# Optimization experiments

Measured on AMD Instinct MI355X. Metric: run time of the kernel, lower is better.

## Reference

```python
import jax, jax.numpy as jnp
import numpy as np
import math

B = 1024
FV = 4096
E = 256
Z = E + 1
EPS = 1e-3
INNER_NSTEP = 8
INNER_LR = 0.5
NS = 16


def setup_inputs() -> dict:
    key = jax.random.key(0)
    ks = jax.random.split(key, 6)
    img = jax.random.uniform(ks[0], (B, FV), dtype=jnp.float32)
    lab = jax.random.randint(ks[1], (B,), 0, 10, dtype=jnp.int64)
    w_dec_w = jax.random.normal(ks[2], (FV, E), dtype=jnp.float32) / np.sqrt(E)
    w_dec_b = jnp.zeros((FV,), dtype=jnp.float32)
    whz_w = jax.random.normal(ks[3], (E, Z), dtype=jnp.float32) / np.sqrt(Z)
    whz_b = jnp.zeros((E,), dtype=jnp.float32)
    b_loc_prior = jax.random.normal(ks[4], (Z,), dtype=jnp.float32) * 0.1
    b_scale_out = jnp.zeros((), dtype=jnp.float32)
    return {"img": img, "lab": lab, "w_dec_w": w_dec_w, "w_dec_b": w_dec_b,
            "whz_w": whz_w, "whz_b": whz_b, "b_loc_prior": b_loc_prior,
            "b_scale_out": b_scale_out}


def reference(img, lab, w_dec_w, w_dec_b, whz_w, whz_b, b_loc_prior, b_scale_out):
    del lab  # unused by loss_joint_lp
    img_flat = img.reshape((img.shape[0], -1))  # [B, FV]
    Bn = img_flat.shape[0]
    node_h = jnp.full((Bn, E), EPS, dtype=img.dtype)
    node_z = jnp.full((Bn, Z), EPS, dtype=img.dtype)
    out_prec = jnp.exp(2.0 * b_scale_out)
    log_prior_sig = jax.nn.log_sigmoid(b_loc_prior)  # [Z]

    def step(carry, k):
        node_h, node_z = carry
        k1, k2 = jax.random.split(k)
        node_e = node_h @ w_dec_w.T + w_dec_b                     # [B, FV]
        dh1 = ((img_flat - node_e) * out_prec) @ w_dec_w          # [B, E]
        h_post_log = node_z @ whz_w.T + whz_b                     # [B, E]
        dh2 = jax.nn.log_sigmoid(h_post_log)
        dz1 = (node_h * jax.nn.sigmoid(-h_post_log)) @ whz_w + log_prior_sig  # [B, Z]
        h_next = jax.nn.sigmoid(dh1 + dh2)
        z_next = jax.nn.sigmoid(dz1)
        sel_h = jax.random.uniform(k1, node_h.shape) < INNER_LR
        sel_z = jax.random.uniform(k2, node_z.shape) < INNER_LR
        node_h = jnp.where(sel_h, 0.5 * (node_h + h_next), node_h)
        node_z = jnp.where(sel_z, 0.5 * (node_z + z_next), node_z)
        node_h = jax.lax.stop_gradient(node_h)  # mirrors .detach()
        node_z = jax.lax.stop_gradient(node_z)
        return (node_h, node_z), None

    loop_keys = jax.random.split(jax.random.key(42), INNER_NSTEP)
    (node_h, node_z), _ = jax.lax.scan(step, (node_h, node_z), loop_keys)

    # Importance-weighted bound with NS Bernoulli samples
    sk = jax.random.split(jax.random.key(7), 2)
    z_noise = (jax.random.uniform(sk[0], (NS, Bn, Z)) < node_z).astype(img.dtype)
    h_post_log = z_noise @ whz_w.T + whz_b                        # [NS, B, E]
    h_noise = (jax.random.uniform(sk[1], (NS, Bn, E)) < jax.nn.sigmoid(h_post_log)).astype(img.dtype)
    loc = h_noise @ w_dec_w.T + w_dec_b                           # [NS, B, FV]

    # Normal(loc, exp(b_scale_out)).log_prob(img_flat)
    inv_scale = jnp.exp(-b_scale_out)
    lp_external = (-0.5 * ((img_flat - loc) * inv_scale) ** 2
                   - b_scale_out - 0.5 * math.log(2.0 * math.pi))  # [NS, B, FV]

    # Bernoulli(logits=b_loc_prior).log_prob - Bernoulli(probs=node_z).log_prob
    lp_prior = z_noise * b_loc_prior - jax.nn.softplus(b_loc_prior)
    lp_post = z_noise * jnp.log(node_z) + (1.0 - z_noise) * jnp.log1p(-node_z)
    lp_internal = lp_prior - lp_post                               # [NS, B, Z]

    joint = lp_internal.sum(-1) + lp_external.sum(-1)              # [NS, B]
    lse = jax.nn.logsumexp(joint, axis=0) - math.log(NS)           # [B]
    return -lse.mean(0)
```

## Files before the change

kernel.cpp:

```cpp
#include <hip/hip_runtime.h>
#include <stdint.h>

#define B_    1024
#define FV_   4096
#define E_    256
#define Z_    257
#define NS_   16
#define NSB_  16384
#define EPS_  1e-3f

typedef __attribute__((ext_vector_type(8))) short short8v;
typedef __attribute__((ext_vector_type(4))) float f32x4;
#define MFMA16(a,b,c) __builtin_amdgcn_mfma_f32_16x16x32_bf16(a,b,c,0,0,0)

__host__ __device__ __forceinline__ uint32_t rotl32(uint32_t v, int r){
  return (v << r) | (v >> (32 - r));
}
__host__ __device__ __forceinline__ void tf2x32(uint32_t k0, uint32_t k1,
    uint32_t x0, uint32_t x1, uint32_t* o0, uint32_t* o1){
  uint32_t ks2 = k0 ^ k1 ^ 0x1BD11BDAu;
  x0 += k0; x1 += k1;
#define TFR(r) { x0 += x1; x1 = rotl32(x1, (r)); x1 ^= x0; }
  TFR(13) TFR(15) TFR(26) TFR(6)
  x0 += k1;  x1 += ks2 + 1u;
  TFR(17) TFR(29) TFR(16) TFR(24)
  x0 += ks2; x1 += k0 + 2u;
  TFR(13) TFR(15) TFR(26) TFR(6)
  x0 += k0;  x1 += k1 + 3u;
  TFR(17) TFR(29) TFR(16) TFR(24)
  x0 += k1;  x1 += ks2 + 4u;
  TFR(13) TFR(15) TFR(26) TFR(6)
  x0 += ks2; x1 += k0 + 5u;
#undef TFR
  *o0 = x0; *o1 = x1;
}
__device__ __forceinline__ uint64_t tf64(uint32_t k0, uint32_t k1, uint32_t c){
  uint32_t a, b; tf2x32(k0, k1, 0u, c, &a, &b);
  return ((uint64_t)b << 32) | (uint64_t)a;
}
__device__ __forceinline__ float u01(uint32_t bits){
  return __uint_as_float((bits >> 9) | 0x3f800000u) - 1.0f;
}
__device__ __forceinline__ float logsigf(float x){
  return fminf(x, 0.f) - __logf(1.f + __expf(-fabsf(x)));
}
__device__ __forceinline__ float sigf(float x){ return 1.f / (1.f + __expf(-x)); }
__device__ __forceinline__ unsigned short f2bf(float f){
  uint32_t b = __float_as_uint(f);
  return (unsigned short)((b + 0x7fffu + ((b >> 16) & 1u)) >> 16);
}
__device__ __forceinline__ float bf2f(unsigned short u){
  return __uint_as_float(((uint32_t)u) << 16);
}

__global__ __launch_bounds__(256) void k_prep(
    const float* __restrict__ img, const float* __restrict__ wb,
    unsigned short* __restrict__ imgb, float* __restrict__ r2,
    const float* __restrict__ W, unsigned short* __restrict__ Wt,
    const float* __restrict__ whz, unsigned short* __restrict__ whzPh,
    unsigned short* __restrict__ whzTPh){
  __shared__ float ld[32][33];
  __shared__ float red[256];
  int bid = blockIdx.x, t = threadIdx.x;
  if (bid < 1024){
    int b = bid;
    float s = 0.f;
#pragma unroll
    for (int i = 0; i < 4; i++){
      int col = t * 4 + i * 1024;
      float4 v = *(const float4*)&img[(size_t)b * FV_ + col];
      float4 wv = *(const float4*)&wb[col];
      float d0 = v.x - wv.x, d1 = v.y - wv.y, d2 = v.z - wv.z, d3 = v.w - wv.w;
      s = fmaf(d0, d0, fmaf(d1, d1, fmaf(d2, d2, fmaf(d3, d3, s))));
      ushort4 o; o.x = f2bf(d0); o.y = f2bf(d1); o.z = f2bf(d2); o.w = f2bf(d3);
      *(ushort4*)&imgb[(size_t)b * FV_ + col] = o;
    }
    red[t] = s; __syncthreads();
    for (int w = 128; w > 0; w >>= 1){ if (t < w) red[t] += red[t + w]; __syncthreads(); }
    if (!t) r2[b] = red[0];
  } else if (bid < 2048){
    int idx = bid - 1024;
    int f0 = (idx & 127) * 32, e0 = (idx >> 7) * 32;
    int tx = t & 31, ty = t >> 5;
#pragma unroll
    for (int sub = 0; sub < 4; sub++){
      int r = ty + 8 * sub;
      ld[r][tx] = W[(size_t)(f0 + r) * 256 + e0 + tx];
    }
    __syncthreads();
#pragma unroll
    for (int sub = 0; sub < 4; sub++){
      int r = ty + 8 * sub;
      Wt[(size_t)(e0 + r) * 4096 + f0 + tx] = f2bf(ld[tx][r]);
    }
  } else {
    int r = bid - 2048;
    if (r < 256){
      for (int z = t; z < 288; z += 256)
        whzPh[(size_t)r * 288 + z] = (z < Z_) ? f2bf(whz[(size_t)r * Z_ + z]) : (unsigned short)0;
    }
    whzTPh[(size_t)r * 256 + t] = (r < Z_) ? f2bf(whz[(size_t)t * Z_ + r]) : (unsigned short)0;
  }
}

__global__ __launch_bounds__(256) void k_gemms(const unsigned short* __restrict__ Wt,
    const unsigned short* __restrict__ imgb,
    float* __restrict__ ataPart, float* __restrict__ ppPart){
  int bid = blockIdx.x;
  int t = threadIdx.x, lane = t & 63, w = t >> 6, l15 = lane & 15, l4 = lane >> 4;
  if (bid < 256){
    int m0 = (bid & 15) * 16;
    size_t kc = (size_t)(bid >> 4) * 256;
    f32x4 acc[4];
#pragma unroll
    for (int q = 0; q < 4; q++) acc[q] = (f32x4){0.f, 0.f, 0.f, 0.f};
    for (int kt = 0; kt < 8; kt++){
      short8v a = *(const short8v*)&Wt[(size_t)(m0 + l15) * 4096 + kc + kt * 32 + l4 * 8];
#pragma unroll
      for (int q = 0; q < 4; q++){
        short8v b = *(const short8v*)&Wt[(size_t)(w * 64 + q * 16 + l15) * 4096 + kc + kt * 32 + l4 * 8];
        acc[q] = MFMA16(a, b, acc[q]);
      }
    }
    float* dst = ataPart + (size_t)(bid >> 4) * 65536;
#pragma unroll
    for (int q = 0; q < 4; q++)
#pragma unroll
      for (int j = 0; j < 4; j++)
        dst[(size_t)(m0 + l4 * 4 + j) * 256 + w * 64 + q * 16 + l15] = acc[q][j];
  } else {
    int idx = bid - 256;
    int m0 = (idx & 31) * 32;
    size_t kc = (size_t)(idx >> 5) * 512;
    f32x4 acc0[4], acc1[4];
#pragma unroll
    for (int q = 0; q < 4; q++){ acc0[q] = (f32x4){0.f,0.f,0.f,0.f}; acc1[q] = (f32x4){0.f,0.f,0.f,0.f}; }
    for (int kt = 0; kt < 16; kt++){
      short8v a0 = *(const short8v*)&imgb[(size_t)(m0 + l15) * 4096 + kc + kt * 32 + l4 * 8];
      short8v a1 = *(const short8v*)&imgb[(size_t)(m0 + 16 + l15) * 4096 + kc + kt * 32 + l4 * 8];
#pragma unroll
      for (int q = 0; q < 4; q++){
        short8v b = *(const short8v*)&Wt[(size_t)(w * 64 + q * 16 + l15) * 4096 + kc + kt * 32 + l4 * 8];
        acc0[q] = MFMA16(a0, b, acc0[q]);
        acc1[q] = MFMA16(a1, b, acc1[q]);
      }
    }
    float* dst = ppPart + (size_t)(idx >> 5) * (B_ * 256);
#pragma unroll
    for (int q = 0; q < 4; q++)
#pragma unroll
      for (int j = 0; j < 4; j++){
        dst[(size_t)(m0 + l4 * 4 + j) * 256 + w * 64 + q * 16 + l15] = acc0[q][j];
        dst[(size_t)(m0 + 16 + l4 * 4 + j) * 256 + w * 64 + q * 16 + l15] = acc1[q][j];
      }
  }
}

__global__ void k_reduce(const float* __restrict__ ataPart, unsigned short* __restrict__ Gh,
                         const float* __restrict__ ppPart, float* __restrict__ Pp){
  int bid = blockIdx.x, t = threadIdx.x;
  if (bid < 256){
    int i = bid * 256 + t;
    float s = 0.f;
#pragma unroll
    for (int p = 0; p < 16; p++) s += ataPart[(size_t)p * 65536 + i];
    Gh[i] = f2bf(s);
  } else {
    int i = (bid - 256) * 256 + t;
    float s = 0.f;
#pragma unroll
    for (int p = 0; p < 8; p++) s += ppPart[(size_t)p * (B_ * 256) + i];
    Pp[i] = s;
  }
}

__global__ __launch_bounds__(512, 1) void k_inner(
    const unsigned short* __restrict__ whzPh,
    const unsigned short* __restrict__ whzTPh,
    const unsigned short* __restrict__ Gh,
    const float* __restrict__ whzb,
    const float* __restrict__ blp,
    const float* __restrict__ Pp,
    const float* __restrict__ bso,
    float* __restrict__ nzOut, float* __restrict__ cA, float* __restrict__ rowB,
    uint32_t hk00, uint32_t hk01, uint32_t hk10, uint32_t hk11,
    uint32_t zk00, uint32_t zk01, uint32_t zk10, uint32_t zk11)
{
  __shared__ unsigned short zb[16][296];
  __shared__ unsigned short hbuf[2][16][296];
  __shared__ unsigned short sgb[16][296];
  __shared__ float zl[16][260];
  __shared__ float ppl[16][256];
  __shared__ float lsb[272];
  __shared__ float xbl[272];
  __shared__ float w256l[256];
  __shared__ uint64_t hbitL[272][2];
  __shared__ uint64_t zbitL[272][2];

  const int t = threadIdx.x;
  const int lane = t & 63;
  const int w = t >> 6;
  const int l15 = lane & 15;
  const int l4 = lane >> 4;
  const int blk = blockIdx.x;
  const int b0 = blk * 16;
  const int n0 = w * 32 + l15;
  const int n1 = n0 + 16;

  const unsigned short epsb = f2bf(EPS_);
  for (int i = t; i < 16 * 296; i += 512){
    int r = i / 296, c = i % 296;
    zb[r][c] = (c < Z_) ? epsb : (unsigned short)0;
    hbuf[0][r][c] = (c < 256) ? epsb : (unsigned short)0;
    hbuf[1][r][c] = 0;
    sgb[r][c] = 0;
  }
  for (int i = t; i < 16 * 260; i += 512){
    int r = i / 260, c = i % 260;
    zl[r][c] = (c < Z_) ? EPS_ : 0.f;
  }
  for (int i = t; i < 4096; i += 512)
    ppl[i >> 8][i & 255] = Pp[(size_t)(b0 + (i >> 8)) * 256 + (i & 255)];
  if (t < 272){
    float x = (t < Z_) ? blp[t] : 0.f;
    xbl[t] = x;
    lsb[t] = logsigf(x);
    hbitL[t][0] = tf64(hk00, hk01, (uint32_t)(blk * 272 + t));
    hbitL[t][1] = tf64(hk10, hk11, (uint32_t)(blk * 272 + t));
    zbitL[t][0] = tf64(zk00, zk01, (uint32_t)(blk * 272 + t));
    zbitL[t][1] = tf64(zk10, zk11, (uint32_t)(blk * 272 + t));
  }
  if (t < 256) w256l[t] = bf2f(whzTPh[(size_t)256 * 256 + t]);

  const unsigned short* wApt0 = &whzPh[(size_t)n0 * 288 + l4 * 8];
  const unsigned short* wApt1 = &whzPh[(size_t)n1 * 288 + l4 * 8];
  const unsigned short* wBpt0 = &Gh[(size_t)n0 * 256 + l4 * 8];
  const unsigned short* wBpt1 = &Gh[(size_t)n1 * 256 + l4 * 8];
  const unsigned short* wCpt0 = &whzTPh[(size_t)n0 * 256 + l4 * 8];
  const unsigned short* wCpt1 = &whzTPh[(size_t)n1 * 256 + l4 * 8];
  const float w256A0 = bf2f(whzPh[(size_t)n0 * 288 + 256]);
  const float w256A1 = bf2f(whzPh[(size_t)n1 * 288 + 256]);
  const float op = __expf(2.f * bso[0]);
  const float wbr0 = whzb[n0], wbr1 = whzb[n1];
  const float lsr0 = logsigf(blp[n0]), lsr1 = logsigf(blp[n1]);
  const float lsr2 = logsigf(blp[256]);
  float hreg0[4] = {EPS_, EPS_, EPS_, EPS_};
  float hreg1[4] = {EPS_, EPS_, EPS_, EPS_};
  __syncthreads();

  for (int s = 0; s < 8; s++){
    const int sg = s >> 2, sh = (s & 3) << 4;
    const int cur = s & 1, nx = cur ^ 1;

    f32x4 aA0 = {0.f, 0.f, 0.f, 0.f};
    {
      short8v wt[8];
#pragma unroll
      for (int kt = 0; kt < 8; kt++) wt[kt] = *(const short8v*)(wApt0 + kt * 32);
#pragma unroll
      for (int kt = 0; kt < 8; kt++)
        aA0 = MFMA16(*(const short8v*)&zb[l15][kt * 32 + l4 * 8], wt[kt], aA0);
    }
    f32x4 aA1 = {0.f, 0.f, 0.f, 0.f};
    {
      short8v wt[8];
#pragma unroll
      for (int kt = 0; kt < 8; kt++) wt[kt] = *(const short8v*)(wApt1 + kt * 32);
#pragma unroll
      for (int kt = 0; kt < 8; kt++)
        aA1 = MFMA16(*(const short8v*)&zb[l15][kt * 32 + l4 * 8], wt[kt], aA1);
    }
    float d2r0[4], d2r1[4];
#pragma unroll
    for (int j = 0; j < 4; j++){
      int m = l4 * 4 + j;
      float z256v = bf2f(zb[m][256]);
      float hpl0 = aA0[j] + wbr0 + z256v * w256A0;
      float hpl1 = aA1[j] + wbr1 + z256v * w256A1;
      d2r0[j] = logsigf(hpl0);
      d2r1[j] = logsigf(hpl1);
      sgb[m][n0] = f2bf(hreg0[j] * sigf(-hpl0));
      sgb[m][n1] = f2bf(hreg1[j] * sigf(-hpl1));
    }
    __syncthreads();

    f32x4 aB0 = {0.f, 0.f, 0.f, 0.f};
    {
      short8v wt[8];
#pragma unroll
      for (int kt = 0; kt < 8; kt++) wt[kt] = *(const short8v*)(wBpt0 + kt * 32);
#pragma unroll
      for (int kt = 0; kt < 8; kt++)
        aB0 = MFMA16(*(const short8v*)&hbuf[cur][l15][kt * 32 + l4 * 8], wt[kt], aB0);
    }
    f32x4 aB1 = {0.f, 0.f, 0.f, 0.f};
    {
      short8v wt[8];
#pragma unroll
      for (int kt = 0; kt < 8; kt++) wt[kt] = *(const short8v*)(wBpt1 + kt * 32);
#pragma unroll
      for (int kt = 0; kt < 8; kt++)
        aB1 = MFMA16(*(const short8v*)&hbuf[cur][l15][kt * 32 + l4 * 8], wt[kt], aB1);
    }
    f32x4 aC0 = {0.f, 0.f, 0.f, 0.f};
    {
      short8v wt[8];
#pragma unroll
      for (int kt = 0; kt < 8; kt++) wt[kt] = *(const short8v*)(wCpt0 + kt * 32);
#pragma unroll
      for (int kt = 0; kt < 8; kt++)
        aC0 = MFMA16(*(const short8v*)&sgb[l15][kt * 32 + l4 * 8], wt[kt], aC0);
    }
    f32x4 aC1 = {0.f, 0.f, 0.f, 0.f};
    {
      short8v wt[8];
#pragma unroll
      for (int kt = 0; kt < 8; kt++) wt[kt] = *(const short8v*)(wCpt1 + kt * 32);
#pragma unroll
      for (int kt = 0; kt < 8; kt++)
        aC1 = MFMA16(*(const short8v*)&sgb[l15][kt * 32 + l4 * 8], wt[kt], aC1);
    }
    float zdot = 0.f;
    if (w == 0){
      int r = lane & 15, kg = lane >> 4;
#pragma unroll
      for (int c = 0; c < 8; c++){
        short8v sv = *(const short8v*)&sgb[r][kg * 64 + c * 8];
#pragma unroll
        for (int i = 0; i < 8; i++)
          zdot = fmaf(bf2f((unsigned short)sv[i]), w256l[kg * 64 + c * 8 + i], zdot);
      }
      zdot += __shfl_xor(zdot, 16);
      zdot += __shfl_xor(zdot, 32);
    }

    {
      uint64_t hb0w = hbitL[n0][sg], hb1w = hbitL[n1][sg];
#pragma unroll
      for (int j = 0; j < 4; j++){
        int m = l4 * 4 + j;
        float hn0 = sigf(op * (ppl[m][n0] - aB0[j]) + d2r0[j]);
        float hn1 = sigf(op * (ppl[m][n1] - aB1[j]) + d2r1[j]);
        if ((hb0w >> (sh | m)) & 1ull) hreg0[j] = 0.5f * (hreg0[j] + hn0);
        if ((hb1w >> (sh | m)) & 1ull) hreg1[j] = 0.5f * (hreg1[j] + hn1);
        hbuf[nx][m][n0] = f2bf(hreg0[j]);
        hbuf[nx][m][n1] = f2bf(hreg1[j]);
      }
    }
    {
      uint64_t zb0w = zbitL[n0][sg], zb1w = zbitL[n1][sg];
#pragma unroll
      for (int j = 0; j < 4; j++){
        int m = l4 * 4 + j;
        float zx0 = sigf(aC0[j] + lsr0);
        float old0 = zl[m][n0];
        float nz0 = ((zb0w >> (sh | m)) & 1ull) ? 0.5f * (old0 + zx0) : old0;
        zl[m][n0] = nz0; zb[m][n0] = f2bf(nz0);
        float zx1 = sigf(aC1[j] + lsr1);
        float old1 = zl[m][n1];
        float nz1 = ((zb1w >> (sh | m)) & 1ull) ? 0.5f * (old1 + zx1) : old1;
        zl[m][n1] = nz1; zb[m][n1] = f2bf(nz1);
      }
    }
    if (w == 0 && lane < 16){
      int r = lane;
      uint64_t zw = zbitL[256][sg];
      float zx = sigf(zdot + lsr2);
      float old = zl[r][256];
      float nz = ((zw >> (sh | r)) & 1ull) ? 0.5f * (old + zx) : old;
      zl[r][256] = nz; zb[r][256] = f2bf(nz);
    }
    __syncthreads();
  }

  {
    int r = t >> 5, g = t & 31;
    float s = 0.f;
    for (int c = g; c < Z_; c += 32){
      float pz = zl[r][c];
      float lgp = __logf(pz);
      float lgq = log1pf(-pz);
      float x = xbl[c];
      nzOut[(size_t)(b0 + r) * Z_ + c] = pz;
      cA[(size_t)(b0 + r) * Z_ + c] = x - lgp + lgq;
      s += -(x - lsb[c]) - lgq;
    }
#pragma unroll
    for (int m = 16; m >= 1; m >>= 1) s += __shfl_xor(s, m);
    if (g == 0) rowB[b0 + r] = s;
  }
}

__global__ __launch_bounds__(256) void k_phase2(
    const float* __restrict__ nzF, const float* __restrict__ cA,
    const float* __restrict__ rowBg,
    const unsigned short* __restrict__ whzPh, const float* __restrict__ whzb,
    const unsigned short* __restrict__ Gh, const float* __restrict__ Pp,
    const float* __restrict__ r2, const float* __restrict__ bso,
    float* __restrict__ joint,
    uint32_t zk0, uint32_t zk1, uint32_t hk0, uint32_t hk1){
  __shared__ unsigned short znl[32][296];
  __shared__ unsigned short hnl[32][264];
  __shared__ float lpl[32];
  __shared__ float sred[4][32][2];

  const int t = threadIdx.x, lane = t & 63, w = t >> 6;
  const int l15 = lane & 15, l4 = lane >> 4;
  const int m0 = blockIdx.x * 32;
  const int bb0 = m0 & (B_ - 1);

  for (int i = t; i < 32 * 32; i += 256){
    znl[i >> 5][256 + (i & 31)] = 0;
  }
  if (t < 32) lpl[t] = rowBg[bb0 + t];
  __syncthreads();

  for (int sub = 0; sub < 16; sub++){
    int rl = sub * 2 + (t >> 7);
    int rg = m0 + rl;
    int b = bb0 + rl;
    int tpos = t & 127;
    uint32_t o0, o1;
    tf2x32(zk0, zk1, 0u, (uint32_t)(rg * 130 + tpos), &o0, &o1);
    int z0 = 2 * tpos;
    float acc = 0.f;
    {
      float pz0 = nzF[(size_t)b * Z_ + z0];
      float pz1 = nzF[(size_t)b * Z_ + z0 + 1];
      int v0 = u01(o0) < pz0;
      int v1 = u01(o1) < pz1;
      uint32_t pack = (v0 ? 0x3F80u : 0u) | (v1 ? 0x3F800000u : 0u);
      *(uint32_t*)&znl[rl][z0] = pack;
      if (v0) acc += cA[(size_t)b * Z_ + z0];
      if (v1) acc += cA[(size_t)b * Z_ + z0 + 1];
    }
    if (tpos == 0){
      uint32_t p0, p1;
      tf2x32(zk0, zk1, 0u, (uint32_t)(rg * 130 + 128), &p0, &p1);
      float pz = nzF[(size_t)b * Z_ + 256];
      int v = u01(p0) < pz;
      znl[rl][256] = v ? (unsigned short)0x3F80 : (unsigned short)0;
      if (v) acc += cA[(size_t)b * Z_ + 256];
    }
// ... 92 lines not shown
        sred[w][16 + l4 * 4 + j][1] = s2b[j];
      }
    }
    __syncthreads();
    if (t < 32){
      float S1 = 0.f, S2 = 0.f;
#pragma unroll
      for (int wv = 0; wv < 4; wv++){ S1 += sred[wv][t][0]; S2 += sred[wv][t][1]; }
      int gm = m0 + t;
      int b = gm & (B_ - 1);
      float bs = bso[0];
      float isc2 = __expf(-2.f * bs);
      float se = r2[b] - 2.f * S2 + S1;
      joint[gm] = lpl[t] - 0.5f * isc2 * se - (float)FV_ * (bs + 0.91893853320467274f);
    }
  }
}

__global__ __launch_bounds__(1024) void k_final(const float* __restrict__ joint, float* __restrict__ out){
  int b = threadIdx.x;
  float mx = -3.0e38f;
  for (int n = 0; n < NS_; n++) mx = fmaxf(mx, joint[(size_t)n * B_ + b]);
  float s = 0.f;
  for (int n = 0; n < NS_; n++) s += __expf(joint[(size_t)n * B_ + b] - mx);
  float lse = mx + __logf(s) - 2.772588722239781f;
  __shared__ float red[1024];
  red[b] = lse; __syncthreads();
  for (int w = 512; w > 0; w >>= 1){ if (b < w) red[b] += red[b + w]; __syncthreads(); }
  if (!b) out[0] = -red[0] / (float)B_;
}

extern "C" void kernel_launch(void* const* d_in, const int* in_sizes, int n_in,
                              void* d_out, int out_size, void* d_ws, size_t ws_size,
                              hipStream_t stream){
  const float* img  = (const float*)d_in[0];
  const float* W    = (const float*)d_in[2];
  const float* wb   = (const float*)d_in[3];
  const float* whz  = (const float*)d_in[4];
  const float* whzb = (const float*)d_in[5];
  const float* blp  = (const float*)d_in[6];
  const float* bso  = (const float*)d_in[7];
  float* out = (float*)d_out;
  float* ws = (float*)d_ws;
  (void)in_sizes; (void)n_in; (void)out_size; (void)ws_size;

  size_t off = 0;
  auto nxt = [&](size_t n){ size_t o = off; off += (n + 63) & ~(size_t)63; return o; };
  float* Pp    = ws + nxt((size_t)B_ * 256);
  float* r2    = ws + nxt(B_);
  float* joint = ws + nxt(NSB_);
  float* nzF   = ws + nxt((size_t)B_ * Z_);
  float* cA    = ws + nxt((size_t)B_ * Z_);
  float* rowB  = ws + nxt(B_);
  unsigned short* Gh     = (unsigned short*)(ws + nxt((size_t)256 * 256 / 2));
  unsigned short* whzPh  = (unsigned short*)(ws + nxt((size_t)256 * 288 / 2));
  unsigned short* whzTPh = (unsigned short*)(ws + nxt((size_t)272 * 256 / 2));
  unsigned short* Wt     = (unsigned short*)(ws + nxt((size_t)256 * 4096 / 2));
  unsigned short* imgb   = (unsigned short*)(ws + nxt((size_t)B_ * FV_ / 2));
  float* ataPart = ws + nxt((size_t)16 * 65536);
  float* ppPart  = ws + nxt((size_t)8 * B_ * 256);

  uint32_t hk00, hk01, hk10, hk11, zk00, zk01, zk10, zk11;
  tf2x32(0u, 42u, 1u, 0u, &hk00, &hk01);
  tf2x32(0u, 42u, 1u, 1u, &hk10, &hk11);
  tf2x32(0u, 42u, 2u, 0u, &zk00, &zk01);
  tf2x32(0u, 42u, 2u, 1u, &zk10, &zk11);
  uint32_t sk00, sk01, sk10, sk11;
  tf2x32(0u, 7u, 0u, 0u, &sk00, &sk01);
  tf2x32(0u, 7u, 0u, 1u, &sk10, &sk11);

  k_prep<<<dim3(2320), 256, 0, stream>>>(img, wb, imgb, r2, W, Wt, whz, whzPh, whzTPh);
  k_gemms<<<dim3(512), 256, 0, stream>>>(Wt, imgb, ataPart, ppPart);
  k_reduce<<<dim3(1280), 256, 0, stream>>>(ataPart, Gh, ppPart, Pp);
  k_inner<<<dim3(64), 512, 0, stream>>>(whzPh, whzTPh, Gh, whzb, blp, Pp, bso,
                                        nzF, cA, rowB,
                                        hk00, hk01, hk10, hk11, zk00, zk01, zk10, zk11);
  k_phase2<<<dim3(512), 256, 0, stream>>>(nzF, cA, rowB, whzPh, whzb, Gh, Pp, r2, bso,
                                          joint, sk00, sk01, sk10, sk11);
  k_final<<<dim3(1), 1024, 0, stream>>>(joint, out);
}
```

Baseline: 133.9 us.

## Process 32 rows per block in inner loop to reuse loaded weight fragments

The inner iterative kernel now handles 32 batch rows per block instead of 16 and launches 32 blocks instead of 64, so each weight fragment loaded from global memory feeds two MFMA row groups. The fp32 state copies (zl, hreg) are dropped and h/z state is kept only as bf16 in shared memory, which also stores Pp as bf16 to fit the larger tile. Log-sigmoid and sigmoid now share one exp. This cuts weight traffic per row, but uses only half as many blocks on a GPU with many CUs, and adds bf16 rounding to the recurrent state, which may shift numerics.

Result: slower. 174.4 us (+30.3%).

```diff
diff --git a/kernel.cpp b/kernel.cpp
--- a/kernel.cpp
+++ b/kernel.cpp
@@ -186,16 +186,15 @@
     uint32_t hk00, uint32_t hk01, uint32_t hk10, uint32_t hk11,
     uint32_t zk00, uint32_t zk01, uint32_t zk10, uint32_t zk11)
 {
-  __shared__ unsigned short zb[16][296];
-  __shared__ unsigned short hbuf[2][16][296];
-  __shared__ unsigned short sgb[16][296];
-  __shared__ float zl[16][260];
-  __shared__ float ppl[16][256];
+  __shared__ unsigned short zb[32][296];
+  __shared__ unsigned short hbuf[2][32][296];
+  __shared__ unsigned short sgb[32][296];
+  __shared__ unsigned short ppl[32][264];
+  __shared__ float w256l[256];
+  __shared__ float xbl[272];
   __shared__ float lsb[272];
-  __shared__ float xbl[272];
-  __shared__ float w256l[256];
-  __shared__ uint64_t hbitL[272][2];
-  __shared__ uint64_t zbitL[272][2];
+  __shared__ uint64_t hbitL[2][272][2];
+  __shared__ uint64_t zbitL[2][272][2];
 
   const int t = threadIdx.x;
   const int lane = t & 63;
@@ -203,32 +202,32 @@
   const int l15 = lane & 15;
   const int l4 = lane >> 4;
   const int blk = blockIdx.x;
-  const int b0 = blk * 16;
+  const int b0 = blk * 32;
   const int n0 = w * 32 + l15;
   const int n1 = n0 + 16;
 
   const unsigned short epsb = f2bf(EPS_);
-  for (int i = t; i < 16 * 296; i += 512){
+  for (int i = t; i < 32 * 296; i += 512){
     int r = i / 296, c = i % 296;
     zb[r][c] = (c < Z_) ? epsb : (unsigned short)0;
     hbuf[0][r][c] = (c < 256) ? epsb : (unsigned short)0;
     hbuf[1][r][c] = 0;
     sgb[r][c] = 0;
   }
-  for (int i = t; i < 16 * 260; i += 512){
-    int r = i / 260, c = i % 260;
-    zl[r][c] = (c < Z_) ? EPS_ : 0.f;
-  }
-  for (int i = t; i < 4096; i += 512)
-    ppl[i >> 8][i & 255] = Pp[(size_t)(b0 + (i >> 8)) * 256 + (i & 255)];
+  for (int i = t; i < 32 * 256; i += 512)
+    ppl[i >> 8][i & 255] = f2bf(Pp[(size_t)(b0 + (i >> 8)) * 256 + (i & 255)]);
+  for (int i = t; i < 2 * 272; i += 512){
+    int g = i / 272, n = i % 272;
+    uint32_t ctr = (uint32_t)((blk * 2 + g) * 272 + n);
+    hbitL[g][n][0] = tf64(hk00, hk01, ctr);
+    hbitL[g][n][1] = tf64(hk10, hk11, ctr);
+    zbitL[g][n][0] = tf64(zk00, zk01, ctr);
+    zbitL[g][n][1] = tf64(zk10, zk11, ctr);
+  }
   if (t < 272){
     float x = (t < Z_) ? blp[t] : 0.f;
     xbl[t] = x;
     lsb[t] = logsigf(x);
-    hbitL[t][0] = tf64(hk00, hk01, (uint32_t)(blk * 272 + t));
-    hbitL[t][1] = tf64(hk10, hk11, (uint32_t)(blk * 272 + t));
-    zbitL[t][0] = tf64(zk00, zk01, (uint32_t)(blk * 272 + t));
-    zbitL[t][1] = tf64(zk10, zk11, (uint32_t)(blk * 272 + t));
   }
   if (t < 256) w256l[t] = bf2f(whzTPh[(size_t)256 * 256 + t]);
 
@@ -244,88 +243,111 @@
   const float wbr0 = whzb[n0], wbr1 = whzb[n1];
   const float lsr0 = logsigf(blp[n0]), lsr1 = logsigf(blp[n1]);
   const float lsr2 = logsigf(blp[256]);
-  float hreg0[4] = {EPS_, EPS_, EPS_, EPS_};
-  float hreg1[4] = {EPS_, EPS_, EPS_, EPS_};
   __syncthreads();
 
   for (int s = 0; s < 8; s++){
     const int sg = s >> 2, sh = (s & 3) << 4;
     const int cur = s & 1, nx = cur ^ 1;
 
-    f32x4 aA0 = {0.f, 0.f, 0.f, 0.f};
+    f32x4 aA0[2] = {{0.f,0.f,0.f,0.f},{0.f,0.f,0.f,0.f}};
     {
       short8v wt[8];
 #pragma unroll
       for (int kt = 0; kt < 8; kt++) wt[kt] = *(const short8v*)(wApt0 + kt * 32);
 #pragma unroll
       for (int kt = 0; kt < 8; kt++)
-        aA0 = MFMA16(*(const short8v*)&zb[l15][kt * 32 + l4 * 8], wt[kt], aA0);
-    }
-    f32x4 aA1 = {0.f, 0.f, 0.f, 0.f};
+#pragma unroll
+        for (int g = 0; g < 2; g++)
+          aA0[g] = MFMA16(*(const short8v*)&zb[g * 16 + l15][kt * 32 + l4 * 8], wt[kt], aA0[g]);
+    }
+    f32x4 aA1[2] = {{0.f,0.f,0.f,0.f},{0.f,0.f,0.f,0.f}};
     {
       short8v wt[8];
 #pragma unroll
       for (int kt = 0; kt < 8; kt++) wt[kt] = *(const short8v*)(wApt1 + kt * 32);
 #pragma unroll
       for (int kt = 0; kt < 8; kt++)
-        aA1 = MFMA16(*(const short8v*)&zb[l15][kt * 32 + l4 * 8], wt[kt], aA1);
-    }
-    float d2r0[4], d2r1[4];
-#pragma unroll
-    for (int j = 0; j < 4; j++){
-      int m = l4 * 4 + j;
-      float z256v = bf2f(zb[m][256]);
-      float hpl0 = aA0[j] + wbr0 + z256v * w256A0;
-      float hpl1 = aA1[j] + wbr1 + z256v * w256A1;
-      d2r0[j] = logsigf(hpl0);
-      d2r1[j] = logsigf(hpl1);
-      sgb[m][n0] = f2bf(hreg0[j] * sigf(-hpl0));
-      sgb[m][n1] = f2bf(hreg1[j] * sigf(-hpl1));
+#pragma unroll
+        for (int g = 0; g < 2; g++)
+          aA1[g] = MFMA16(*(const short8v*)&zb[g * 16 + l15][kt * 32 + l4 * 8], wt[kt], aA1[g]);
+    }
+    float d2r0[2][4], d2r1[2][4];
+#pragma unroll
+    for (int g = 0; g < 2; g++){
+#pragma unroll
+      for (int j = 0; j < 4; j++){
+        int m = g * 16 + l4 * 4 + j;
+        float z256v = bf2f(zb[m][256]);
+        {
+          float hpl = aA0[g][j] + wbr0 + z256v * w256A0;
+          float e = __expf(-fabsf(hpl));
+          float den = 1.f + e;
+          d2r0[g][j] = fminf(hpl, 0.f) - __logf(den);
+          float sgv = (hpl >= 0.f ? e : 1.f) / den;
+          sgb[m][n0] = f2bf(bf2f(hbuf[cur][m][n0]) * sgv);
+        }
+        {
+          float hpl = aA1[g][j] + wbr1 + z256v * w256A1;
+          float e = __expf(-fabsf(hpl));
+          float den = 1.f + e;
+          d2r1[g][j] = fminf(hpl, 0.f) - __logf(den);
+          float sgv = (hpl >= 0.f ? e : 1.f) / den;
+          sgb[m][n1] = f2bf(bf2f(hbuf[cur][m][n1]) * sgv);
+        }
+      }
     }
     __syncthreads();
 
-    f32x4 aB0 = {0.f, 0.f, 0.f, 0.f};
+    f32x4 aB0[2] = {{0.f,0.f,0.f,0.f},{0.f,0.f,0.f,0.f}};
     {
       short8v wt[8];
 #pragma unroll
       for (int kt = 0; kt < 8; kt++) wt[kt] = *(const short8v*)(wBpt0 + kt * 32);
 #pragma unroll
       for (int kt = 0; kt < 8; kt++)
-        aB0 = MFMA16(*(const short8v*)&hbuf[cur][l15][kt * 32 + l4 * 8], wt[kt], aB0);
-    }
-    f32x4 aB1 = {0.f, 0.f, 0.f, 0.f};
+#pragma unroll
+        for (int g = 0; g < 2; g++)
+          aB0[g] = MFMA16(*(const short8v*)&hbuf[cur][g * 16 + l15][kt * 32 + l4 * 8], wt[kt], aB0[g]);
+    }
+    f32x4 aB1[2] = {{0.f,0.f,0.f,0.f},{0.f,0.f,0.f,0.f}};
     {
       short8v wt[8];
 #pragma unroll
       for (int kt = 0; kt < 8; kt++) wt[kt] = *(const short8v*)(wBpt1 + kt * 32);
 #pragma unroll
       for (int kt = 0; kt < 8; kt++)
-        aB1 = MFMA16(*(const short8v*)&hbuf[cur][l15][kt * 32 + l4 * 8], wt[kt], aB1);
-    }
-    f32x4 aC0 = {0.f, 0.f, 0.f, 0.f};
+#pragma unroll
+        for (int g = 0; g < 2; g++)
+          aB1[g] = MFMA16(*(const short8v*)&hbuf[cur][g * 16 + l15][kt * 32 + l4 * 8], wt[kt], aB1[g]);
+    }
+    f32x4 aC0[2] = {{0.f,0.f,0.f,0.f},{0.f,0.f,0.f,0.f}};
     {
       short8v wt[8];
 #pragma unroll
       for (int kt = 0; kt < 8; kt++) wt[kt] = *(const short8v*)(wCpt0 + kt * 32);
 #pragma unroll
       for (int kt = 0; kt < 8; kt++)
-        aC0 = MFMA16(*(const short8v*)&sgb[l15][kt * 32 + l4 * 8], wt[kt], aC0);
-    }
-    f32x4 aC1 = {0.f, 0.f, 0.f, 0.f};
+#pragma unroll
+        for (int g = 0; g < 2; g++)
+          aC0[g] = MFMA16(*(const short8v*)&sgb[g * 16 + l15][kt * 32 + l4 * 8], wt[kt], aC0[g]);
+    }
+    f32x4 aC1[2] = {{0.f,0.f,0.f,0.f},{0.f,0.f,0.f,0.f}};
     {
       short8v wt[8];
 #pragma unroll
       for (int kt = 0; kt < 8; kt++) wt[kt] = *(const short8v*)(wCpt1 + kt * 32);
 #pragma unroll
       for (int kt = 0; kt < 8; kt++)
-        aC1 = MFMA16(*(const short8v*)&sgb[l15][kt * 32 + l4 * 8], wt[kt], aC1);
+#pragma unroll
+        for (int g = 0; g < 2; g++)
+          aC1[g] = MFMA16(*(const short8v*)&sgb[g * 16 + l15][kt * 32 + l4 * 8], wt[kt], aC1[g]);
     }
     float zdot = 0.f;
-    if (w == 0){
+    if (w < 2){
       int r = lane & 15, kg = lane >> 4;
 #pragma unroll
       for (int c = 0; c < 8; c++){
-        short8v sv = *(const short8v*)&sgb[r][kg * 64 + c * 8];
+        short8v sv = *(const short8v*)&sgb[w * 16 + r][kg * 64 + c * 8];
 #pragma unroll
         for (int i = 0; i < 8; i++)
           zdot = fmaf(bf2f((unsigned short)sv[i]), w256l[kg * 64 + c * 8 + i], zdot);
@@ -334,60 +356,65 @@
       zdot += __shfl_xor(zdot, 32);
     }
 
-    {
-      uint64_t hb0w = hbitL[n0][sg], hb1w = hbitL[n1][sg];
+#pragma unroll
+    for (int g = 0; g < 2; g++){
+      uint64_t hb0 = hbitL[g][n0][sg], hb1 = hbitL[g][n1][sg];
 #pragma unroll
       for (int j = 0; j < 4; j++){
-        int m = l4 * 4 + j;
-        float hn0 = sigf(op * (ppl[m][n0] - aB0[j]) + d2r0[j]);
-        float hn1 = sigf(op * (ppl[m][n1] - aB1[j]) + d2r1[j]);
-        if ((hb0w >> (sh | m)) & 1ull) hreg0[j] = 0.5f * (hreg0[j] + hn0);
-        if ((hb1w >> (sh | m)) & 1ull) hreg1[j] = 0.5f * (hreg1[j] + hn1);
-        hbuf[nx][m][n0] = f2bf(hreg0[j]);
-        hbuf[nx][m][n1] = f2bf(hreg1[j]);
-      }
-    }
-    {
-      uint64_t zb0w = zbitL[n0][sg], zb1w = zbitL[n1][sg];
+        int ml = l4 * 4 + j;
+        int m = g * 16 + ml;
+        float old0 = bf2f(hbuf[cur][m][n0]);
+        float hn0 = sigf(op * (bf2f(ppl[m][n0]) - aB0[g][j]) + d2r0[g][j]);
+        float nh0 = ((hb0 >> (sh | ml)) & 1ull) ? 0.5f * (old0 + hn0) : old0;
+        hbuf[nx][m][n0] = f2bf(nh0);
+        float old1 = bf2f(hbuf[cur][m][n1]);
+        float hn1 = sigf(op * (bf2f(ppl[m][n1]) - aB1[g][j]) + d2r1[g][j]);
+        float nh1 = ((hb1 >> (sh | ml)) & 1ull) ? 0.5f * (old1 + hn1) : old1;
+        hbuf[nx][m][n1] = f2bf(nh1);
+      }
+    }
+#pragma unroll
+    for (int g = 0; g < 2; g++){
+      uint64_t zb0w = zbitL[g][n0][sg], zb1w = zbitL[g][n1][sg];
 #pragma unroll
       for (int j = 0; j < 4; j++){
-        int m = l4 * 4 + j;
-        float zx0 = sigf(aC0[j] + lsr0);
-        float old0 = zl[m][n0];
-        float nz0 = ((zb0w >> (sh | m)) & 1ull) ? 0.5f * (old0 + zx0) : old0;
-        zl[m][n0] = nz0; zb[m][n0] = f2bf(nz0);
-        float zx1 = sigf(aC1[j] + lsr1);
-        float old1 = zl[m][n1];
-        float nz1 = ((zb1w >> (sh | m)) & 1ull) ? 0.5f * (old1 + zx1) : old1;
-        zl[m][n1] = nz1; zb[m][n1] = f2bf(nz1);
-      }
-    }
-    if (w == 0 && lane < 16){
+        int ml = l4 * 4 + j;
+        int m = g * 16 + ml;
+        float old0 = bf2f(zb[m][n0]);
+        float zx0 = sigf(aC0[g][j] + lsr0);
+        float nz0 = ((zb0w >> (sh | ml)) & 1ull) ? 0.5f * (old0 + zx0) : old0;
+        zb[m][n0] = f2bf(nz0);
+        float old1 = bf2f(zb[m][n1]);
+        float zx1 = sigf(aC1[g][j] + lsr1);
+        float nz1 = ((zb1w >> (sh | ml)) & 1ull) ? 0.5f * (old1 + zx1) : old1;
+        zb[m][n1] = f2bf(nz1);
+      }
+    }
+    if (w < 2 && lane < 16){
       int r = lane;
-      uint64_t zw = zbitL[256][sg];
+      uint64_t zw = zbitL[w][256][sg];
+      float old = bf2f(zb[w * 16 + r][256]);
       float zx = sigf(zdot + lsr2);
-      float old = zl[r][256];
       float nz = ((zw >> (sh | r)) & 1ull) ? 0.5f * (old + zx) : old;
-      zl[r][256] = nz; zb[r][256] = f2bf(nz);
+      zb[w * 16 + r][256] = f2bf(nz);
     }
     __syncthreads();
   }
 
   {
-    int r = t >> 5, g = t & 31;
+    int rl = t >> 4, g16 = t & 15;
     float s = 0.f;
-    for (int c = g; c < Z_; c += 32){
-      float pz = zl[r][c];
-      float lgp = __logf(pz);
+    for (int c = g16; c < Z_; c += 16){
+      float pz = bf2f(zb[rl][c]);
       float lgq = log1pf(-pz);
       float x = xbl[c];
-      nzOut[(size_t)(b0 + r) * Z_ + c] = pz;
-      cA[(size_t)(b0 + r) * Z_ + c] = x - lgp + lgq;
+      nzOut[(size_t)(b0 + rl) * Z_ + c] = pz;
+      cA[(size_t)(b0 + rl) * Z_ + c] = x - __logf(pz) + lgq;
       s += -(x - lsb[c]) - lgq;
     }
 #pragma unroll
-    for (int m = 16; m >= 1; m >>= 1) s += __shfl_xor(s, m);
-    if (g == 0) rowB[b0 + r] = s;
+    for (int msk = 1; msk < 16; msk <<= 1) s += __shfl_xor(s, msk);
+    if (g16 == 0) rowB[b0 + rl] = s;
   }
 }
 
@@ -607,7 +634,7 @@
   k_prep<<<dim3(2320), 256, 0, stream>>>(img, wb, imgb, r2, W, Wt, whz, whzPh, whzTPh);
   k_gemms<<<dim3(512), 256, 0, stream>>>(Wt, imgb, ataPart, ppPart);
   k_reduce<<<dim3(1280), 256, 0, stream>>>(ataPart, Gh, ppPart, Pp);
-  k_inner<<<dim3(64), 512, 0, stream>>>(whzPh, whzTPh, Gh, whzb, blp, Pp, bso,
+  k_inner<<<dim3(32), 512, 0, stream>>>(whzPh, whzTPh, Gh, whzb, blp, Pp, bso,
                                         nzF, cA, rowB,
                                         hk00, hk01, hk10, hk11, zk00, zk01, zk10, zk11);
   k_phase2<<<dim3(512), 256, 0, stream>>>(nzF, cA, rowB, whzPh, whzb, Gh, Pp, r2, bso,
```

## Split persistent inner-loop kernel into per-step launches over more blocks

Applied to the files above, without the earlier changes.

The single 64-block persistent kernel for the 8 inner iterations is replaced by two kernels per step (stepA and stepB), each launched with 256 blocks, plus a tail kernel for the final z statistics. The h, z and intermediate sigmoid buffers now live in global memory and are initialized in extra k_prep blocks. The aim is to use many more CUs than the 64 the old grid could occupy. The cost is 16 extra launches and global round trips of state each step. z is also now kept only in bf16 instead of an fp32 shadow copy, which lowers precision.

After: 180.2 us. 1.35x slower.

```diff
diff --git a/kernel.cpp b/kernel.cpp
--- a/kernel.cpp
+++ b/kernel.cpp
@@ -58,10 +58,12 @@
     unsigned short* __restrict__ imgb, float* __restrict__ r2,
     const float* __restrict__ W, unsigned short* __restrict__ Wt,
     const float* __restrict__ whz, unsigned short* __restrict__ whzPh,
-    unsigned short* __restrict__ whzTPh){
+    unsigned short* __restrict__ whzTPh,
+    unsigned short* __restrict__ zG, unsigned short* __restrict__ hG){
   __shared__ float ld[32][33];
   __shared__ float red[256];
   int bid = blockIdx.x, t = threadIdx.x;
+  const unsigned short epsb = f2bf(EPS_);
   if (bid < 1024){
     int b = bid;
     float s = 0.f;
@@ -93,13 +95,25 @@
       int r = ty + 8 * sub;
       Wt[(size_t)(e0 + r) * 4096 + f0 + tx] = f2bf(ld[tx][r]);
     }
-  } else {
+  } else if (bid < 2320){
     int r = bid - 2048;
     if (r < 256){
       for (int z = t; z < 288; z += 256)
         whzPh[(size_t)r * 288 + z] = (z < Z_) ? f2bf(whz[(size_t)r * Z_ + z]) : (unsigned short)0;
     }
     whzTPh[(size_t)r * 256 + t] = (r < Z_) ? f2bf(whz[(size_t)t * Z_ + r]) : (unsigned short)0;
+  } else if (bid < 2576){
+    int r0 = (bid - 2320) * 4;
+    for (int idx = t; idx < 4 * 288; idx += 256){
+      int r = r0 + idx / 288, c = idx % 288;
+      zG[(size_t)r * 288 + c] = (c < Z_) ? epsb : (unsigned short)0;
+    }
+  } else {
+    int r0 = (bid - 2576) * 4;
+    for (int idx = t; idx < 4 * 256; idx += 256){
+      int r = r0 + (idx >> 8), c = idx & 255;
+      hG[(size_t)r * 256 + c] = epsb;
+    }
   }
 }
 
@@ -174,221 +188,127 @@
   }
 }
 
-__global__ __launch_bounds__(512, 1) void k_inner(
+__global__ __launch_bounds__(256) void k_stepA(
+    const unsigned short* __restrict__ zG,
+    const unsigned short* __restrict__ hcur,
     const unsigned short* __restrict__ whzPh,
-    const unsigned short* __restrict__ whzTPh,
-    const unsigned short* __restrict__ Gh,
     const float* __restrict__ whzb,
-    const float* __restrict__ blp,
-    const float* __restrict__ Pp,
+    unsigned short* __restrict__ sgbG,
+    float* __restrict__ d2G)
+{
+  const int t = threadIdx.x, lane = t & 63, w = t >> 6;
+  const int l15 = lane & 15, l4 = lane >> 4;
+  const int rowblk = blockIdx.x >> 2, cg = blockIdx.x & 3;
+  const int row0 = rowblk * 16;
+  const int n = cg * 64 + w * 16 + l15;
+
+  f32x4 acc = {0.f, 0.f, 0.f, 0.f};
+#pragma unroll
+  for (int kt = 0; kt < 9; kt++){
+    short8v za = *(const short8v*)&zG[(size_t)(row0 + l15) * 288 + kt * 32 + l4 * 8];
+    short8v wa = *(const short8v*)&whzPh[(size_t)n * 288 + kt * 32 + l4 * 8];
+    acc = MFMA16(za, wa, acc);
+  }
+  const float wbv = whzb[n];
+#pragma unroll
+  for (int j = 0; j < 4; j++){
+    int row = row0 + l4 * 4 + j;
+    float hpl = acc[j] + wbv;
+    float e = __expf(-fabsf(hpl));
+    float den = 1.f + e;
+    float d2 = fminf(hpl, 0.f) - __logf(den);
+    float sgv = (hpl >= 0.f ? e : 1.f) / den;
+    float hv = bf2f(hcur[(size_t)row * 256 + n]);
+    sgbG[(size_t)row * 256 + n] = f2bf(hv * sgv);
+    d2G[(size_t)row * 256 + n] = d2;
+  }
+}
+
+__global__ __launch_bounds__(256) void k_stepB(
+    const unsigned short* __restrict__ hcur, unsigned short* __restrict__ hnxt,
+    unsigned short* __restrict__ zG,
+    const unsigned short* __restrict__ sgbG, const float* __restrict__ d2G,
+    const unsigned short* __restrict__ Gh, const unsigned short* __restrict__ whzTPh,
+    const float* __restrict__ Pp, const float* __restrict__ blp,
     const float* __restrict__ bso,
-    float* __restrict__ nzOut, float* __restrict__ cA, float* __restrict__ rowB,
-    uint32_t hk00, uint32_t hk01, uint32_t hk10, uint32_t hk11,
-    uint32_t zk00, uint32_t zk01, uint32_t zk10, uint32_t zk11)
+    uint32_t hk0, uint32_t hk1, uint32_t zk0, uint32_t zk1, int sh)
 {
-  __shared__ unsigned short zb[16][296];
-  __shared__ unsigned short hbuf[2][16][296];
-  __shared__ unsigned short sgb[16][296];
-  __shared__ float zl[16][260];
-  __shared__ float ppl[16][256];
-  __shared__ float lsb[272];
-  __shared__ float xbl[272];
-  __shared__ float w256l[256];
-  __shared__ uint64_t hbitL[272][2];
-  __shared__ uint64_t zbitL[272][2];
-
-  const int t = threadIdx.x;
-  const int lane = t & 63;
-  const int w = t >> 6;
-  const int l15 = lane & 15;
-  const int l4 = lane >> 4;
-  const int blk = blockIdx.x;
-  const int b0 = blk * 16;
-  const int n0 = w * 32 + l15;
-  const int n1 = n0 + 16;
-
-  const unsigned short epsb = f2bf(EPS_);
-  for (int i = t; i < 16 * 296; i += 512){
-    int r = i / 296, c = i % 296;
-    zb[r][c] = (c < Z_) ? epsb : (unsigned short)0;
-    hbuf[0][r][c] = (c < 256) ? epsb : (unsigned short)0;
-    hbuf[1][r][c] = 0;
-    sgb[r][c] = 0;
-  }
-  for (int i = t; i < 16 * 260; i += 512){
-    int r = i / 260, c = i % 260;
-    zl[r][c] = (c < Z_) ? EPS_ : 0.f;
-  }
-  for (int i = t; i < 4096; i += 512)
-    ppl[i >> 8][i & 255] = Pp[(size_t)(b0 + (i >> 8)) * 256 + (i & 255)];
-  if (t < 272){
-    float x = (t < Z_) ? blp[t] : 0.f;
-    xbl[t] = x;
-    lsb[t] = logsigf(x);
-    hbitL[t][0] = tf64(hk00, hk01, (uint32_t)(blk * 272 + t));
-    hbitL[t][1] = tf64(hk10, hk11, (uint32_t)(blk * 272 + t));
-    zbitL[t][0] = tf64(zk00, zk01, (uint32_t)(blk * 272 + t));
-    zbitL[t][1] = tf64(zk10, zk11, (uint32_t)(blk * 272 + t));
-  }
-  if (t < 256) w256l[t] = bf2f(whzTPh[(size_t)256 * 256 + t]);
-
-  const unsigned short* wApt0 = &whzPh[(size_t)n0 * 288 + l4 * 8];
-  const unsigned short* wApt1 = &whzPh[(size_t)n1 * 288 + l4 * 8];
-  const unsigned short* wBpt0 = &Gh[(size_t)n0 * 256 + l4 * 8];
-  const unsigned short* wBpt1 = &Gh[(size_t)n1 * 256 + l4 * 8];
-  const unsigned short* wCpt0 = &whzTPh[(size_t)n0 * 256 + l4 * 8];
-  const unsigned short* wCpt1 = &whzTPh[(size_t)n1 * 256 + l4 * 8];
-  const float w256A0 = bf2f(whzPh[(size_t)n0 * 288 + 256]);
-  const float w256A1 = bf2f(whzPh[(size_t)n1 * 288 + 256]);
+  const int t = threadIdx.x, lane = t & 63, w = t >> 6;
+  const int l15 = lane & 15, l4 = lane >> 4;
+  const int rowblk = blockIdx.x >> 2, cg = blockIdx.x & 3;
+  const int row0 = rowblk * 16;
+  const int n = cg * 64 + w * 16 + l15;
+
+  f32x4 aB = {0.f,0.f,0.f,0.f}, aC = {0.f,0.f,0.f,0.f};
+#pragma unroll
+  for (int kt = 0; kt < 8; kt++){
+    short8v ha = *(const short8v*)&hcur[(size_t)(row0 + l15) * 256 + kt * 32 + l4 * 8];
+    short8v wg = *(const short8v*)&Gh[(size_t)n * 256 + kt * 32 + l4 * 8];
+    aB = MFMA16(ha, wg, aB);
+    short8v sa = *(const short8v*)&sgbG[(size_t)(row0 + l15) * 256 + kt * 32 + l4 * 8];
+    short8v wc = *(const short8v*)&whzTPh[(size_t)n * 256 + kt * 32 + l4 * 8];
+    aC = MFMA16(sa, wc, aC);
+  }
   const float op = __expf(2.f * bso[0]);
-  const float wbr0 = whzb[n0], wbr1 = whzb[n1];
-  const float lsr0 = logsigf(blp[n0]), lsr1 = logsigf(blp[n1]);
-  const float lsr2 = logsigf(blp[256]);
-  float hreg0[4] = {EPS_, EPS_, EPS_, EPS_};
-  float hreg1[4] = {EPS_, EPS_, EPS_, EPS_};
-  __syncthreads();
-
-  for (int s = 0; s < 8; s++){
-    const int sg = s >> 2, sh = (s & 3) << 4;
-    const int cur = s & 1, nx = cur ^ 1;
-
-    f32x4 aA0 = {0.f, 0.f, 0.f, 0.f};
-    {
-      short8v wt[8];
-#pragma unroll
-      for (int kt = 0; kt < 8; kt++) wt[kt] = *(const short8v*)(wApt0 + kt * 32);
-#pragma unroll
-      for (int kt = 0; kt < 8; kt++)
-        aA0 = MFMA16(*(const short8v*)&zb[l15][kt * 32 + l4 * 8], wt[kt], aA0);
-    }
-    f32x4 aA1 = {0.f, 0.f, 0.f, 0.f};
-    {
-      short8v wt[8];
-#pragma unroll
-      for (int kt = 0; kt < 8; kt++) wt[kt] = *(const short8v*)(wApt1 + kt * 32);
-#pragma unroll
-      for (int kt = 0; kt < 8; kt++)
-        aA1 = MFMA16(*(const short8v*)&zb[l15][kt * 32 + l4 * 8], wt[kt], aA1);
-    }
-    float d2r0[4], d2r1[4];
-#pragma unroll
-    for (int j = 0; j < 4; j++){
-      int m = l4 * 4 + j;
-      float z256v = bf2f(zb[m][256]);
-      float hpl0 = aA0[j] + wbr0 + z256v * w256A0;
-      float hpl1 = aA1[j] + wbr1 + z256v * w256A1;
-      d2r0[j] = logsigf(hpl0);
-      d2r1[j] = logsigf(hpl1);
-      sgb[m][n0] = f2bf(hreg0[j] * sigf(-hpl0));
-      sgb[m][n1] = f2bf(hreg1[j] * sigf(-hpl1));
-    }
-    __syncthreads();
-
-    f32x4 aB0 = {0.f, 0.f, 0.f, 0.f};
-    {
-      short8v wt[8];
-#pragma unroll
-      for (int kt = 0; kt < 8; kt++) wt[kt] = *(const short8v*)(wBpt0 + kt * 32);
-#pragma unroll
-      for (int kt = 0; kt < 8; kt++)
-        aB0 = MFMA16(*(const short8v*)&hbuf[cur][l15][kt * 32 + l4 * 8], wt[kt], aB0);
-    }
-    f32x4 aB1 = {0.f, 0.f, 0.f, 0.f};
-    {
-      short8v wt[8];
-#pragma unroll
-      for (int kt = 0; kt < 8; kt++) wt[kt] = *(const short8v*)(wBpt1 + kt * 32);
-#pragma unroll
-      for (int kt = 0; kt < 8; kt++)
-        aB1 = MFMA16(*(const short8v*)&hbuf[cur][l15][kt * 32 + l4 * 8], wt[kt], aB1);
-    }
-    f32x4 aC0 = {0.f, 0.f, 0.f, 0.f};
-    {
-      short8v wt[8];
-#pragma unroll
-      for (int kt = 0; kt < 8; kt++) wt[kt] = *(const short8v*)(wCpt0 + kt * 32);
-#pragma unroll
-      for (int kt = 0; kt < 8; kt++)
-        aC0 = MFMA16(*(const short8v*)&sgb[l15][kt * 32 + l4 * 8], wt[kt], aC0);
-    }
-    f32x4 aC1 = {0.f, 0.f, 0.f, 0.f};
-    {
-      short8v wt[8];
-#pragma unroll
-      for (int kt = 0; kt < 8; kt++) wt[kt] = *(const short8v*)(wCpt1 + kt * 32);
-#pragma unroll
-      for (int kt = 0; kt < 8; kt++)
-        aC1 = MFMA16(*(const short8v*)&sgb[l15][kt * 32 + l4 * 8], wt[kt], aC1);
-    }
-    float zdot = 0.f;
-    if (w == 0){
-      int r = lane & 15, kg = lane >> 4;
-#pragma unroll
-      for (int c = 0; c < 8; c++){
-        short8v sv = *(const short8v*)&sgb[r][kg * 64 + c * 8];
-#pragma unroll
-        for (int i = 0; i < 8; i++)
-          zdot = fmaf(bf2f((unsigned short)sv[i]), w256l[kg * 64 + c * 8 + i], zdot);
-      }
-      zdot += __shfl_xor(zdot, 16);
-      zdot += __shfl_xor(zdot, 32);
-    }
-
-    {
-      uint64_t hb0w = hbitL[n0][sg], hb1w = hbitL[n1][sg];
+  const float lsr = logsigf(blp[n]);
+  uint64_t hb = tf64(hk0, hk1, (uint32_t)(rowblk * 272 + n));
+  uint64_t zbw = tf64(zk0, zk1, (uint32_t)(rowblk * 272 + n));
+#pragma unroll
+  for (int j = 0; j < 4; j++){
+    int m = l4 * 4 + j;
+    int row = row0 + m;
+    float old = bf2f(hcur[(size_t)row * 256 + n]);
+    float hn = sigf(op * (Pp[(size_t)row * 256 + n] - aB[j]) + d2G[(size_t)row * 256 + n]);
+    float nh = ((hb >> (sh | m)) & 1ull) ? 0.5f * (old + hn) : old;
+    hnxt[(size_t)row * 256 + n] = f2bf(nh);
+    float zold = bf2f(zG[(size_t)row * 288 + n]);
+    float zx = sigf(aC[j] + lsr);
+    float nz = ((zbw >> (sh | m)) & 1ull) ? 0.5f * (zold + zx) : zold;
+    zG[(size_t)row * 288 + n] = f2bf(nz);
+  }
+  if (cg == 0 && w == 0){
+    f32x4 aC2 = {0.f,0.f,0.f,0.f};
+#pragma unroll
+    for (int kt = 0; kt < 8; kt++){
+      short8v sa = *(const short8v*)&sgbG[(size_t)(row0 + l15) * 256 + kt * 32 + l4 * 8];
+      short8v wc2 = *(const short8v*)&whzTPh[(size_t)(256 + l15) * 256 + kt * 32 + l4 * 8];
+      aC2 = MFMA16(sa, wc2, aC2);
+    }
+    if (l15 == 0){
+      float lsr2 = logsigf(blp[256]);
+      uint64_t zb2 = tf64(zk0, zk1, (uint32_t)(rowblk * 272 + 256));
 #pragma unroll
       for (int j = 0; j < 4; j++){
         int m = l4 * 4 + j;
-        float hn0 = sigf(op * (ppl[m][n0] - aB0[j]) + d2r0[j]);
-        float hn1 = sigf(op * (ppl[m][n1] - aB1[j]) + d2r1[j]);
-        if ((hb0w >> (sh | m)) & 1ull) hreg0[j] = 0.5f * (hreg0[j] + hn0);
-        if ((hb1w >> (sh | m)) & 1ull) hreg1[j] = 0.5f * (hreg1[j] + hn1);
-        hbuf[nx][m][n0] = f2bf(hreg0[j]);
-        hbuf[nx][m][n1] = f2bf(hreg1[j]);
-      }
-    }
-    {
-      uint64_t zb0w = zbitL[n0][sg], zb1w = zbitL[n1][sg];
-#pragma unroll
-      for (int j = 0; j < 4; j++){
-        int m = l4 * 4 + j;
-        float zx0 = sigf(aC0[j] + lsr0);
-        float old0 = zl[m][n0];
-        float nz0 = ((zb0w >> (sh | m)) & 1ull) ? 0.5f * (old0 + zx0) : old0;
-        zl[m][n0] = nz0; zb[m][n0] = f2bf(nz0);
-        float zx1 = sigf(aC1[j] + lsr1);
-        float old1 = zl[m][n1];
-        float nz1 = ((zb1w >> (sh | m)) & 1ull) ? 0.5f * (old1 + zx1) : old1;
-        zl[m][n1] = nz1; zb[m][n1] = f2bf(nz1);
-      }
-    }
-    if (w == 0 && lane < 16){
-      int r = lane;
-      uint64_t zw = zbitL[256][sg];
-      float zx = sigf(zdot + lsr2);
-      float old = zl[r][256];
-      float nz = ((zw >> (sh | r)) & 1ull) ? 0.5f * (old + zx) : old;
-      zl[r][256] = nz; zb[r][256] = f2bf(nz);
-    }
-    __syncthreads();
-  }
-
-  {
-    int r = t >> 5, g = t & 31;
-    float s = 0.f;
-    for (int c = g; c < Z_; c += 32){
-      float pz = zl[r][c];
-      float lgp = __logf(pz);
-      float lgq = log1pf(-pz);
-      float x = xbl[c];
-      nzOut[(size_t)(b0 + r) * Z_ + c] = pz;
-      cA[(size_t)(b0 + r) * Z_ + c] = x - lgp + lgq;
-      s += -(x - lsb[c]) - lgq;
-    }
-#pragma unroll
-    for (int m = 16; m >= 1; m >>= 1) s += __shfl_xor(s, m);
-    if (g == 0) rowB[b0 + r] = s;
-  }
+        int row = row0 + m;
+        float zold = bf2f(zG[(size_t)row * 288 + 256]);
+        float zx = sigf(aC2[j] + lsr2);
+        float nz = ((zb2 >> (sh | m)) & 1ull) ? 0.5f * (zold + zx) : zold;
+        zG[(size_t)row * 288 + 256] = f2bf(nz);
+      }
+    }
+  }
+}
+
+__global__ __launch_bounds__(256) void k_tail(const unsigned short* __restrict__ zG,
+    const float* __restrict__ blp, float* __restrict__ nzF, float* __restrict__ cA,
+    float* __restrict__ rowB){
+  int blk = blockIdx.x, t = threadIdx.x;
+  int rl = t >> 4, g16 = t & 15;
+  int row = blk * 16 + rl;
+  float s = 0.f;
+  for (int c = g16; c < Z_; c += 16){
+    float pz = bf2f(zG[(size_t)row * 288 + c]);
+    float lgq = log1pf(-pz);
+    float x = blp[c];
+    float ls = logsigf(x);
+    nzF[(size_t)row * Z_ + c] = pz;
+    cA[(size_t)row * Z_ + c] = x - __logf(pz) + lgq;
+    s += -(x - ls) - lgq;
+  }
+#pragma unroll
+  for (int msk = 1; msk < 16; msk <<= 1) s += __shfl_xor(s, msk);
+  if (g16 == 0) rowB[row] = s;
 }
 
 __global__ __launch_bounds__(256) void k_phase2(
@@ -587,11 +507,16 @@
   float* nzF   = ws + nxt((size_t)B_ * Z_);
   float* cA    = ws + nxt((size_t)B_ * Z_);
   float* rowB  = ws + nxt(B_);
+  float* d2G   = ws + nxt((size_t)B_ * 256);
   unsigned short* Gh     = (unsigned short*)(ws + nxt((size_t)256 * 256 / 2));
   unsigned short* whzPh  = (unsigned short*)(ws + nxt((size_t)256 * 288 / 2));
   unsigned short* whzTPh = (unsigned short*)(ws + nxt((size_t)272 * 256 / 2));
   unsigned short* Wt     = (unsigned short*)(ws + nxt((size_t)256 * 4096 / 2));
   unsigned short* imgb   = (unsigned short*)(ws + nxt((size_t)B_ * FV_ / 2));
+  unsigned short* zG     = (unsigned short*)(ws + nxt((size_t)B_ * 288 / 2));
+  unsigned short* hA     = (unsigned short*)(ws + nxt((size_t)B_ * 256 / 2));
+  unsigned short* hB     = (unsigned short*)(ws + nxt((size_t)B_ * 256 / 2));
+  unsigned short* sgbG   = (unsigned short*)(ws + nxt((size_t)B_ * 256 / 2));
   float* ataPart = ws + nxt((size_t)16 * 65536);
   float* ppPart  = ws + nxt((size_t)8 * B_ * 256);
 
@@ -604,12 +529,22 @@
   tf2x32(0u, 7u, 0u, 0u, &sk00, &sk01);
   tf2x32(0u, 7u, 0u, 1u, &sk10, &sk11);
 
-  k_prep<<<dim3(2320), 256, 0, stream>>>(img, wb, imgb, r2, W, Wt, whz, whzPh, whzTPh);
+  k_prep<<<dim3(2832), 256, 0, stream>>>(img, wb, imgb, r2, W, Wt, whz, whzPh, whzTPh, zG, hA);
   k_gemms<<<dim3(512), 256, 0, stream>>>(Wt, imgb, ataPart, ppPart);
   k_reduce<<<dim3(1280), 256, 0, stream>>>(ataPart, Gh, ppPart, Pp);
-  k_inner<<<dim3(64), 512, 0, stream>>>(whzPh, whzTPh, Gh, whzb, blp, Pp, bso,
-                                        nzF, cA, rowB,
-                                        hk00, hk01, hk10, hk11, zk00, zk01, zk10, zk11);
+
+  for (int s = 0; s < 8; s++){
+    unsigned short* hcur = (s & 1) ? hB : hA;
+    unsigned short* hnxt = (s & 1) ? hA : hB;
+    k_stepA<<<dim3(256), 256, 0, stream>>>(zG, hcur, whzPh, whzb, sgbG, d2G);
+    uint32_t hk0 = (s < 4) ? hk00 : hk10, hk1 = (s < 4) ? hk01 : hk11;
+    uint32_t zk0 = (s < 4) ? zk00 : zk10, zk1 = (s < 4) ? zk01 : zk11;
+    int sh = (s & 3) << 4;
+    k_stepB<<<dim3(256), 256, 0, stream>>>(hcur, hnxt, zG, sgbG, d2G, Gh, whzTPh,
+                                           Pp, blp, bso, hk0, hk1, zk0, zk1, sh);
+  }
+
+  k_tail<<<dim3(64), 256, 0, stream>>>(zG, blp, nzF, cA, rowB);
   k_phase2<<<dim3(512), 256, 0, stream>>>(nzF, cA, rowB, whzPh, whzb, Gh, Pp, r2, bso,
                                           joint, sk00, sk01, sk10, sk11);
   k_final<<<dim3(1), 1024, 0, stream>>>(joint, out);
```
